# Kernel tuning notes

Measured on AMD Instinct MI355X. Metric: run time of the kernel, lower is better.

## Reference

```python
import jax, jax.numpy as jnp
import numpy as np

HEADS = 16
DIMS = [64, 64, 64, 64]  # [d_att(Q), d_att(K), d_ff(V), d_ff(G)]
EPS = 1e-4
P_POW = 2


def _cdist(Q, K):
    # Euclidean pairwise distance via the norm expansion, like torch.cdist.
    # Q: [h, b, t, d], K: [h, b, t, d] -> [h, b, t, t]
    q2 = jnp.sum(Q * Q, axis=-1)  # [h, b, t]
    k2 = jnp.sum(K * K, axis=-1)  # [h, b, t]
    qk = jnp.einsum('hbtd,hbsd->hbts', Q, K)
    d2 = q2[..., :, None] + k2[..., None, :] - 2.0 * qk
    return jnp.sqrt(jnp.maximum(d2, 0.0))


def setup_inputs() -> dict:
    key = jax.random.key(0)
    ks = jax.random.split(key, 4)
    b, t, d_in = 2, 2048, 1024
    d_proj = HEADS * sum(DIMS)  # 4096
    X = jax.random.normal(ks[0], (b, t, d_in), dtype=jnp.float32)
    W_in = jax.random.normal(ks[1], (d_in, d_proj), dtype=jnp.float32) * (d_in ** -0.5)
    b_in = jnp.zeros((d_proj,), dtype=jnp.float32)
    W_out = jax.random.normal(ks[2], (HEADS * DIMS[2], d_in), dtype=jnp.float32) * ((HEADS * DIMS[2]) ** -0.5)
    b_out = jnp.zeros((d_in,), dtype=jnp.float32)
    return {"X": X, "W_in": W_in, "b_in": b_in, "W_out": W_out, "b_out": b_out}


def reference(X, W_in, b_in, W_out, b_out):
    b, t, _ = X.shape
    # multi-head input projection: [b,t,d_in] -> [h,b,t,sum(DIMS)] -> split
    P = X @ W_in + b_in                       # [b, t, h*sum(DIMS)]
    P = P.reshape(b, t, HEADS, sum(DIMS))
    P = jnp.transpose(P, (2, 0, 1, 3))        # [h, b, t, sum(DIMS)]
    splits = np.cumsum(DIMS)[:-1]
    Q, K, V, G = jnp.split(P, splits, axis=-1)
    # Shepard's attention: inverse-power-distance weights
    W = jnp.power(EPS + _cdist(Q, K), -P_POW)         # [h, b, t, t]
    W = W / (EPS + jnp.sum(W, axis=-1, keepdims=True))
    A = jnp.einsum('hbts,hbse->hbte', W, V)           # [h, b, t, e]
    H = G * A                                          # gating
    H = jnp.transpose(H, (1, 2, 0, 3)).reshape(b, t, HEADS * DIMS[2])
    return H @ W_out + b_out
```

## Files before the change

### kernel.cpp

```cpp
#include <hip/hip_runtime.h>
#include <hip/hip_bf16.h>
#include <cstdint>
#include <cstddef>

typedef __bf16 bf16_t;
typedef __attribute__((ext_vector_type(8))) __bf16 bf16x8;
typedef __attribute__((ext_vector_type(4))) __bf16 bf16x4;
typedef __attribute__((ext_vector_type(4))) float f32x4;
typedef __attribute__((ext_vector_type(16))) float f32x16;
typedef __attribute__((ext_vector_type(4))) unsigned int u32x4;

#define ATT_EPS 1e-4f

__device__ __forceinline__ f32x4 mfma_bf16(bf16x8 a, bf16x8 b, f32x4 c) {
  return __builtin_amdgcn_mfma_f32_16x16x32_bf16(a, b, c, 0, 0, 0);
}
__device__ __forceinline__ f32x16 mfma32(bf16x8 a, bf16x8 b, f32x16 c) {
  return __builtin_amdgcn_mfma_f32_32x32x16_bf16(a, b, c, 0, 0, 0);
}
__device__ __forceinline__ unsigned cvtpk_bf16(float lo, float hi) {
  unsigned r;
  asm("v_cvt_pk_bf16_f32 %0, %1, %2" : "=v"(r) : "v"(lo), "v"(hi));
  return r;
}

#define GLDS16(g, l)                                                          \
  __builtin_amdgcn_global_load_lds(                                           \
      (const __attribute__((address_space(1))) void*)(g),                     \
      (__attribute__((address_space(3))) void*)(l), 16, 0, 0)

__global__ __launch_bounds__(256) void cvt_x_kernel(
    const float* __restrict__ X, bf16_t* __restrict__ Xb, int n8) {
  int i = blockIdx.x * 256 + threadIdx.x;
  if (i >= n8) return;
  f32x4 a = ((const f32x4*)X)[i * 2 + 0];
  f32x4 b = ((const f32x4*)X)[i * 2 + 1];
  bf16x8 o;
  o[0] = (__bf16)a[0]; o[1] = (__bf16)a[1]; o[2] = (__bf16)a[2]; o[3] = (__bf16)a[3];
  o[4] = (__bf16)b[0]; o[5] = (__bf16)b[1]; o[6] = (__bf16)b[2]; o[7] = (__bf16)b[3];
  ((bf16x8*)Xb)[i] = o;
}

__global__ __launch_bounds__(256) void tcvt_kernel(
    const float* __restrict__ W, bf16_t* __restrict__ Wt, int R, int C) {
  __shared__ float T[64][65];
  int tx = threadIdx.x & 63, ty = threadIdx.x >> 6;
  int c0 = blockIdx.x * 64, r0 = blockIdx.y * 64;
#pragma unroll
  for (int i = 0; i < 16; ++i) {
    int rr = ty * 16 + i;
    T[rr][tx] = W[(size_t)(r0 + rr) * C + c0 + tx];
  }
  __syncthreads();
#pragma unroll
  for (int i = 0; i < 16; ++i) {
    int cc = ty * 16 + i;
    Wt[(size_t)(c0 + cc) * R + r0 + tx] = (bf16_t)T[tx][cc];
  }
}

__global__ __launch_bounds__(256) void vt_kernel(
    const bf16_t* __restrict__ P, bf16_t* __restrict__ VtG) {
  __shared__ float T[64][65];
  int h = blockIdx.x;
  int r0 = blockIdx.y * 64;
  int tx = threadIdx.x & 63, ty = threadIdx.x >> 6;
  const bf16_t* src = P + (size_t)r0 * 4096 + h * 256 + 128;
#pragma unroll
  for (int i = 0; i < 16; ++i) {
    int rr = ty * 16 + i;
    T[rr][tx] = (float)src[(size_t)rr * 4096 + tx];
  }
  __syncthreads();
#pragma unroll
  for (int i = 0; i < 16; ++i) {
    int cc = ty * 16 + i;
    VtG[(size_t)(h * 64 + cc) * 4096 + r0 + tx] = (bf16_t)T[tx][cc];
  }
}

template <int OUTF32>
__global__ __launch_bounds__(256, 2) void gemm_kernel(
    const bf16_t* __restrict__ A, const bf16_t* __restrict__ Bt,
    const float* __restrict__ bias, void* __restrict__ Cout,
    int M, int N, int K) {
  __shared__ bf16_t As[2][128 * 64];
  __shared__ bf16_t Bs[2][128 * 64];
  int tid = threadIdx.x, lane = tid & 63, wv = tid >> 6;
  int l15 = lane & 15, lhi = lane >> 4;
  int NT = N >> 7;
  int nwg = gridDim.x;
  int qq = nwg >> 3;
  int swz = (blockIdx.x & 7) * qq + (blockIdx.x >> 3);
  int tm = swz / NT, tn = swz % NT;
  int m0 = tm << 7, n0 = tn << 7;
  int wm = (wv >> 1) << 6, wn = (wv & 1) << 6;
  int KT = K >> 6;

  auto stage = [&](int buf, int kt) {
    int k0 = kt << 6;
#pragma unroll
    for (int s = 0; s < 4; ++s) {
      int t = s * 256 + tid;
      int row = t >> 3, u = t & 7;
      int cc = (u ^ (row & 7)) << 3;
      GLDS16(A + (size_t)(m0 + row) * K + k0 + cc, &As[buf][t * 8]);
    }
#pragma unroll
    for (int s = 0; s < 4; ++s) {
      int t = s * 256 + tid;
      int row = t >> 3, u = t & 7;
      int cc = (u ^ (row & 7)) << 3;
      GLDS16(Bt + (size_t)(n0 + row) * K + k0 + cc, &Bs[buf][t * 8]);
    }
  };

  f32x4 zero = {0.f, 0.f, 0.f, 0.f};
  f32x4 acc[4][4];
#pragma unroll
  for (int ms = 0; ms < 4; ++ms)
#pragma unroll
    for (int ns = 0; ns < 4; ++ns) acc[ms][ns] = zero;

  stage(0, 0);
  __syncthreads();
  int cur = 0;
  for (int kt = 0; kt < KT; ++kt) {
    if (kt + 1 < KT) stage(cur ^ 1, kt + 1);
#pragma unroll
    for (int ks = 0; ks < 2; ++ks) {
      bf16x8 af[4], bfr[4];
#pragma unroll
      for (int ms = 0; ms < 4; ++ms) {
        int row = wm + ms * 16 + l15;
        af[ms] = *(const bf16x8*)&As[cur][row * 64 + (((ks * 4 + lhi) ^ (row & 7)) << 3)];
      }
#pragma unroll
      for (int ns = 0; ns < 4; ++ns) {
        int col = wn + ns * 16 + l15;
        bfr[ns] = *(const bf16x8*)&Bs[cur][col * 64 + (((ks * 4 + lhi) ^ (col & 7)) << 3)];
      }
#pragma unroll
      for (int ms = 0; ms < 4; ++ms)
#pragma unroll
        for (int ns = 0; ns < 4; ++ns)
          acc[ms][ns] = mfma_bf16(af[ms], bfr[ns], acc[ms][ns]);
    }
    __syncthreads();
    cur ^= 1;
  }

#pragma unroll
  for (int ns = 0; ns < 4; ++ns) {
    int col = n0 + wn + ns * 16 + l15;
    float bv = bias[col];
#pragma unroll
    for (int ms = 0; ms < 4; ++ms) {
      int rowb = m0 + wm + ms * 16 + lhi * 4;
#pragma unroll
      for (int r = 0; r < 4; ++r) {
        float v = acc[ms][ns][r] + bv;
        if (OUTF32)
          ((float*)Cout)[(size_t)(rowb + r) * N + col] = v;
        else
          ((bf16_t*)Cout)[(size_t)(rowb + r) * N + col] = (bf16_t)v;
      }
    }
  }
}

__global__ __launch_bounds__(256) void norms_kernel(
    const bf16_t* __restrict__ P, float* __restrict__ Q2, float* __restrict__ K2) {
  int tid = threadIdx.x, lane = tid & 63, wv = tid >> 6;
  int wg = blockIdx.x * 4 + wv;
  int h = wg >> 9, rb = wg & 511;
  int r = rb * 8 + (lane >> 3), ch = lane & 7;
  const bf16_t* base = P + (size_t)r * 4096 + h * 256 + ch * 8;
  bf16x8 qv = *(const bf16x8*)base;
  bf16x8 kv = *(const bf16x8*)(base + 64);
  float sq = 0.f, sk = 0.f;
#pragma unroll
  for (int j = 0; j < 8; ++j) {
    float a = (float)qv[j];
    sq += a * a;
    float c = (float)kv[j];
    sk += c * c;
  }
#pragma unroll
  for (int m = 1; m <= 4; m <<= 1) {
    sq += __shfl_xor(sq, m);
    sk += __shfl_xor(sk, m);
  }
  if (ch == 0) {
    Q2[h * 4096 + r] = sq;
    K2[h * 4096 + r] = sk;
  }
}

__global__ __launch_bounds__(256, 3) void attn_kernel(
    const bf16_t* __restrict__ P, const bf16_t* __restrict__ VtG,
    const float* __restrict__ Q2, const float* __restrict__ K2,
    bf16_t* __restrict__ H) {
  __shared__ bf16_t Ks[128 * 64];
  __shared__ bf16_t Vts[64 * 128];
  __shared__ float invLds[4][32];

  int tid = threadIdx.x, lane = tid & 63, wv = tid >> 6;
  int l31 = lane & 31, hi = lane >> 5, hi4 = hi * 4;
  bool hiSel = (hi != 0);
  int swz = (blockIdx.x & 7) * 64 + (blockIdx.x >> 3);
  int hb = swz >> 4, qt = swz & 15;
  int h = hb >> 1, b = hb & 1;
  int rowbase = b * 2048;
  const bf16_t* Pq = P + (size_t)rowbase * 4096 + h * 256;
  const bf16_t* Pk = Pq + 64;
  const bf16_t* Pg = Pq + 192;
  const bf16_t* Vg = VtG + (size_t)h * 64 * 4096 + rowbase;
  const float* Q2g = Q2 + h * 4096 + rowbase;
  const float* K2g = K2 + h * 4096 + rowbase;
  int q0 = qt * 128 + wv * 32;

  bf16x8 qm[4];
#pragma unroll
  for (int db = 0; db < 4; ++db) {
    bf16x8 q = *(const bf16x8*)(Pq + (size_t)(q0 + l31) * 4096 + db * 16 + hi * 8);
    u32x4 u = *(u32x4*)&q;
    u = (u ^ 0x80008000u) + 0x00800080u;
    qm[db] = *(bf16x8*)&u;
  }
  float q2s = Q2g[q0 + l31];

  f32x16 nacc0, nacc1;
#pragma unroll
  for (int r = 0; r < 16; ++r) { nacc0[r] = 0.f; nacc1[r] = 0.f; }
  float dacc0 = 0.f, dacc1 = 0.f;

  for (int st = 0; st < 16; ++st) {
    int s0 = st * 128;
    __syncthreads();
#pragma unroll
    for (int s4 = 0; s4 < 4; ++s4) {
      int t = s4 * 256 + tid;
      int row = t >> 3, u = t & 7;
      int cc = (u ^ (row & 7)) << 3;
      GLDS16(Pk + (size_t)(s0 + row) * 4096 + cc, &Ks[t * 8]);
    }
#pragma unroll
    for (int s4 = 0; s4 < 4; ++s4) {
      int t = s4 * 256 + tid;
      int row = t >> 4, u = t & 15;
      int cc = (u ^ (row & 7)) << 3;
      GLDS16(Vg + (size_t)row * 4096 + s0 + cc, &Vts[t * 8]);
    }
    __syncthreads();

    const float* K2t = K2g + s0;
#pragma unroll
    for (int sb = 0; sb < 4; ++sb) {
      f32x16 D;
#pragma unroll
      for (int g = 0; g < 4; ++g) {
        f32x4 k2v = *(const f32x4*)(K2t + sb * 32 + g * 8 + hi4);
#pragma unroll
        for (int j = 0; j < 4; ++j) D[g * 4 + j] = k2v[j] + q2s;
      }
#pragma unroll
      for (int db = 0; db < 4; ++db) {
        int srow = sb * 32 + l31;
        bf16x8 kf = *(const bf16x8*)&Ks[srow * 64 + (((db * 2 + hi) ^ (srow & 7)) << 3)];
        D = mfma32(kf, qm[db], D);
      }
      float p[16];
#pragma unroll
      for (int r = 0; r < 16; ++r) {
        float w = __builtin_amdgcn_rcpf(fmaxf(D[r], 1e-12f));
        if (r & 1) dacc1 += w; else dacc0 += w;
        p[r] = w;
      }
      unsigned t01 = cvtpk_bf16(p[0], p[1]),  t23 = cvtpk_bf16(p[2], p[3]);
      unsigned t45 = cvtpk_bf16(p[4], p[5]),  t67 = cvtpk_bf16(p[6], p[7]);
      unsigned t89 = cvtpk_bf16(p[8], p[9]),  tab = cvtpk_bf16(p[10], p[11]);
      unsigned tcd = cvtpk_bf16(p[12], p[13]), tef = cvtpk_bf16(p[14], p[15]);
      unsigned x01 = __shfl_xor(t01, 32), x23 = __shfl_xor(t23, 32);
      unsigned x45 = __shfl_xor(t45, 32), x67 = __shfl_xor(t67, 32);
      unsigned x89 = __shfl_xor(t89, 32), xab = __shfl_xor(tab, 32);
      unsigned xcd = __shfl_xor(tcd, 32), xef = __shfl_xor(tef, 32);
      u32x4 w0v = {hiSel ? x45 : t01, hiSel ? x67 : t23,
                   hiSel ? t45 : x01, hiSel ? t67 : x23};
      u32x4 w1v = {hiSel ? xcd : t89, hiSel ? xef : tab,
                   hiSel ? tcd : x89, hiSel ? tef : xab};
      bf16x8 pa0 = *(bf16x8*)&w0v;
      bf16x8 pa1 = *(bf16x8*)&w1v;
      int e = l31;
      {
        int c0 = ((sb * 4 + 0 + hi) ^ (e & 7)) << 3;
        int c1 = ((sb * 4 + 2 + hi) ^ (e & 7)) << 3;
        bf16x8 vb00 = *(const bf16x8*)&Vts[e * 128 + c0];
        bf16x8 vb01 = *(const bf16x8*)&Vts[(e + 32) * 128 + (((sb * 4 + 0 + hi) ^ ((e + 32) & 7)) << 3)];
        bf16x8 vb10 = *(const bf16x8*)&Vts[e * 128 + c1];
        bf16x8 vb11 = *(const bf16x8*)&Vts[(e + 32) * 128 + (((sb * 4 + 2 + hi) ^ ((e + 32) & 7)) << 3)];
        nacc0 = mfma32(pa0, vb00, nacc0);
        nacc1 = mfma32(pa0, vb01, nacc1);
        nacc0 = mfma32(pa1, vb10, nacc0);
        nacc1 = mfma32(pa1, vb11, nacc1);
      }
    }
  }

  float dacc = dacc0 + dacc1;
  dacc += __shfl_xor(dacc, 32);
  float inv = __builtin_amdgcn_rcpf(ATT_EPS + dacc);
  if (lane < 32) invLds[wv][l31] = inv;
  __builtin_amdgcn_s_waitcnt(0);
#pragma unroll
  for (int r = 0; r < 16; ++r) {
    int q = (r & 3) + 8 * (r >> 2) + hi4;
    int tq = q0 + q;
    float iv = invLds[wv][q];
    float g0 = (float)Pg[(size_t)tq * 4096 + l31];
    float g1 = (float)Pg[(size_t)tq * 4096 + 32 + l31];
    H[(size_t)(rowbase + tq) * 1024 + h * 64 + l31] = (bf16_t)(g0 * nacc0[r] * iv);
    H[(size_t)(rowbase + tq) * 1024 + h * 64 + 32 + l31] = (bf16_t)(g1 * nacc1[r] * iv);
  }
}

extern "C" void kernel_launch(void* const* d_in, const int* in_sizes, int n_in,
                              void* d_out, int out_size, void* d_ws, size_t ws_size,
                              hipStream_t stream) {
  const float* X     = (const float*)d_in[0];
  const float* W_in  = (const float*)d_in[1];
  const float* b_in  = (const float*)d_in[2];
  const float* W_out = (const float*)d_in[3];
  const float* b_out = (const float*)d_in[4];

  char* ws = (char*)d_ws;
  bf16_t* Xb  = (bf16_t*)(ws);
  bf16_t* VtG = (bf16_t*)(ws);
  bf16_t* WbT = (bf16_t*)(ws + ((size_t)8  << 20));
  bf16_t* WoT = (bf16_t*)(ws + ((size_t)16 << 20));
  bf16_t* Pb  = (bf16_t*)(ws + ((size_t)18 << 20));
  bf16_t* Hb  = (bf16_t*)(ws + ((size_t)50 << 20));
  float*  Q2  = (float*) (ws + ((size_t)58 << 20));
  float*  K2  = (float*) (ws + ((size_t)59 << 20));

  cvt_x_kernel<<<2048, 256, 0, stream>>>(X, Xb, 4096 * 1024 / 8);
  tcvt_kernel<<<dim3(64, 16), 256, 0, stream>>>(W_in, WbT, 1024, 4096);
  tcvt_kernel<<<dim3(16, 16), 256, 0, stream>>>(W_out, WoT, 1024, 1024);
  gemm_kernel<0><<<1024, 256, 0, stream>>>(Xb, WbT, b_in, Pb, 4096, 4096, 1024);
  norms_kernel<<<2048, 256, 0, stream>>>(Pb, Q2, K2);
  vt_kernel<<<dim3(16, 64), 256, 0, stream>>>(Pb, VtG);
  attn_kernel<<<512, 256, 0, stream>>>(Pb, VtG, Q2, K2, Hb);
  gemm_kernel<1><<<256, 256, 0, stream>>>(Hb, WoT, b_out, d_out, 4096, 1024, 1024);
}
```

Measured before the change: 157.9 us.

## Split attention key tiles across two wave groups and drop P-fragment shuffles

```diff
diff --git a/kernel.cpp b/kernel.cpp
--- a/kernel.cpp
+++ b/kernel.cpp
@@ -5,7 +5,6 @@
 
 typedef __bf16 bf16_t;
 typedef __attribute__((ext_vector_type(8))) __bf16 bf16x8;
-typedef __attribute__((ext_vector_type(4))) __bf16 bf16x4;
 typedef __attribute__((ext_vector_type(4))) float f32x4;
 typedef __attribute__((ext_vector_type(16))) float f32x16;
 typedef __attribute__((ext_vector_type(4))) unsigned int u32x4;
@@ -72,10 +71,11 @@
     T[rr][tx] = (float)src[(size_t)rr * 4096 + tx];
   }
   __syncthreads();
+  int ptx = (tx & ~15) | ((tx & 3) | ((tx & 4) << 1) | ((tx & 8) >> 1));
 #pragma unroll
   for (int i = 0; i < 16; ++i) {
     int cc = ty * 16 + i;
-    VtG[(size_t)(h * 64 + cc) * 4096 + r0 + tx] = (bf16_t)T[tx][cc];
+    VtG[(size_t)(h * 64 + cc) * 4096 + r0 + ptx] = (bf16_t)T[tx][cc];
   }
 }
 
@@ -197,17 +197,19 @@
   }
 }
 
-__global__ __launch_bounds__(256, 3) void attn_kernel(
+__global__ __launch_bounds__(512, 4) void attn_kernel(
     const bf16_t* __restrict__ P, const bf16_t* __restrict__ VtG,
     const float* __restrict__ Q2, const float* __restrict__ K2,
     bf16_t* __restrict__ H) {
   __shared__ bf16_t Ks[128 * 64];
   __shared__ bf16_t Vts[64 * 128];
+  __shared__ float Comb[4][64][33];
   __shared__ float invLds[4][32];
 
   int tid = threadIdx.x, lane = tid & 63, wv = tid >> 6;
   int l31 = lane & 31, hi = lane >> 5, hi4 = hi * 4;
-  bool hiSel = (hi != 0);
+  int qw = wv & 3, sw = wv >> 2;
+  int sOff = sw * 64;
   int swz = (blockIdx.x & 7) * 64 + (blockIdx.x >> 3);
   int hb = swz >> 4, qt = swz & 15;
   int h = hb >> 1, b = hb & 1;
@@ -218,7 +220,7 @@
   const bf16_t* Vg = VtG + (size_t)h * 64 * 4096 + rowbase;
   const float* Q2g = Q2 + h * 4096 + rowbase;
   const float* K2g = K2 + h * 4096 + rowbase;
-  int q0 = qt * 128 + wv * 32;
+  int q0 = qt * 128 + qw * 32;
 
   bf16x8 qm[4];
 #pragma unroll
@@ -239,34 +241,40 @@
     int s0 = st * 128;
     __syncthreads();
 #pragma unroll
-    for (int s4 = 0; s4 < 4; ++s4) {
-      int t = s4 * 256 + tid;
+    for (int s4 = 0; s4 < 2; ++s4) {
+      int t = s4 * 512 + tid;
       int row = t >> 3, u = t & 7;
       int cc = (u ^ (row & 7)) << 3;
       GLDS16(Pk + (size_t)(s0 + row) * 4096 + cc, &Ks[t * 8]);
     }
 #pragma unroll
-    for (int s4 = 0; s4 < 4; ++s4) {
-      int t = s4 * 256 + tid;
+    for (int s4 = 0; s4 < 2; ++s4) {
+      int t = s4 * 512 + tid;
       int row = t >> 4, u = t & 15;
       int cc = (u ^ (row & 7)) << 3;
       GLDS16(Vg + (size_t)row * 4096 + s0 + cc, &Vts[t * 8]);
     }
+    const float* K2t = K2g + s0 + sOff;
+    f32x4 k2a[4];
+#pragma unroll
+    for (int g = 0; g < 4; ++g) k2a[g] = *(const f32x4*)(K2t + g * 8 + hi4);
     __syncthreads();
 
-    const float* K2t = K2g + s0;
-#pragma unroll
-    for (int sb = 0; sb < 4; ++sb) {
+#pragma unroll
+    for (int sb = 0; sb < 2; ++sb) {
+      int sbase = sOff + sb * 32;
       f32x16 D;
 #pragma unroll
-      for (int g = 0; g < 4; ++g) {
-        f32x4 k2v = *(const f32x4*)(K2t + sb * 32 + g * 8 + hi4);
-#pragma unroll
-        for (int j = 0; j < 4; ++j) D[g * 4 + j] = k2v[j] + q2s;
+      for (int g = 0; g < 4; ++g)
+#pragma unroll
+        for (int j = 0; j < 4; ++j) D[g * 4 + j] = k2a[g][j] + q2s;
+      if (sb == 0) {
+#pragma unroll
+        for (int g = 0; g < 4; ++g) k2a[g] = *(const f32x4*)(K2t + 32 + g * 8 + hi4);
       }
 #pragma unroll
       for (int db = 0; db < 4; ++db) {
-        int srow = sb * 32 + l31;
+        int srow = sbase + l31;
         bf16x8 kf = *(const bf16x8*)&Ks[srow * 64 + (((db * 2 + hi) ^ (srow & 7)) << 3)];
         D = mfma32(kf, qm[db], D);
       }
@@ -277,50 +285,56 @@
         if (r & 1) dacc1 += w; else dacc0 += w;
         p[r] = w;
       }
-      unsigned t01 = cvtpk_bf16(p[0], p[1]),  t23 = cvtpk_bf16(p[2], p[3]);
-      unsigned t45 = cvtpk_bf16(p[4], p[5]),  t67 = cvtpk_bf16(p[6], p[7]);
-      unsigned t89 = cvtpk_bf16(p[8], p[9]),  tab = cvtpk_bf16(p[10], p[11]);
-      unsigned tcd = cvtpk_bf16(p[12], p[13]), tef = cvtpk_bf16(p[14], p[15]);
-      unsigned x01 = __shfl_xor(t01, 32), x23 = __shfl_xor(t23, 32);
-      unsigned x45 = __shfl_xor(t45, 32), x67 = __shfl_xor(t67, 32);
-      unsigned x89 = __shfl_xor(t89, 32), xab = __shfl_xor(tab, 32);
-      unsigned xcd = __shfl_xor(tcd, 32), xef = __shfl_xor(tef, 32);
-      u32x4 w0v = {hiSel ? x45 : t01, hiSel ? x67 : t23,
-                   hiSel ? t45 : x01, hiSel ? t67 : x23};
-      u32x4 w1v = {hiSel ? xcd : t89, hiSel ? xef : tab,
-                   hiSel ? tcd : x89, hiSel ? tef : xab};
+      u32x4 w0v = {cvtpk_bf16(p[0], p[1]), cvtpk_bf16(p[2], p[3]),
+                   cvtpk_bf16(p[4], p[5]), cvtpk_bf16(p[6], p[7])};
+      u32x4 w1v = {cvtpk_bf16(p[8], p[9]), cvtpk_bf16(p[10], p[11]),
+                   cvtpk_bf16(p[12], p[13]), cvtpk_bf16(p[14], p[15])};
       bf16x8 pa0 = *(bf16x8*)&w0v;
       bf16x8 pa1 = *(bf16x8*)&w1v;
       int e = l31;
-      {
-        int c0 = ((sb * 4 + 0 + hi) ^ (e & 7)) << 3;
-        int c1 = ((sb * 4 + 2 + hi) ^ (e & 7)) << 3;
-        bf16x8 vb00 = *(const bf16x8*)&Vts[e * 128 + c0];
-        bf16x8 vb01 = *(const bf16x8*)&Vts[(e + 32) * 128 + (((sb * 4 + 0 + hi) ^ ((e + 32) & 7)) << 3)];
-        bf16x8 vb10 = *(const bf16x8*)&Vts[e * 128 + c1];
-        bf16x8 vb11 = *(const bf16x8*)&Vts[(e + 32) * 128 + (((sb * 4 + 2 + hi) ^ ((e + 32) & 7)) << 3)];
-        nacc0 = mfma32(pa0, vb00, nacc0);
-        nacc1 = mfma32(pa0, vb01, nacc1);
-        nacc0 = mfma32(pa1, vb10, nacc0);
-        nacc1 = mfma32(pa1, vb11, nacc1);
-      }
-    }
-  }
-
-  float dacc = dacc0 + dacc1;
-  dacc += __shfl_xor(dacc, 32);
-  float inv = __builtin_amdgcn_rcpf(ATT_EPS + dacc);
-  if (lane < 32) invLds[wv][l31] = inv;
-  __builtin_amdgcn_s_waitcnt(0);
-#pragma unroll
-  for (int r = 0; r < 16; ++r) {
-    int q = (r & 3) + 8 * (r >> 2) + hi4;
-    int tq = q0 + q;
-    float iv = invLds[wv][q];
-    float g0 = (float)Pg[(size_t)tq * 4096 + l31];
-    float g1 = (float)Pg[(size_t)tq * 4096 + 32 + l31];
-    H[(size_t)(rowbase + tq) * 1024 + h * 64 + l31] = (bf16_t)(g0 * nacc0[r] * iv);
-    H[(size_t)(rowbase + tq) * 1024 + h * 64 + 32 + l31] = (bf16_t)(g1 * nacc1[r] * iv);
+      int ciB = (sOff >> 3) + sb * 4;
+      bf16x8 vb00 = *(const bf16x8*)&Vts[e * 128 + (((ciB + 0 + hi) ^ (e & 7)) << 3)];
+      bf16x8 vb01 = *(const bf16x8*)&Vts[(e + 32) * 128 + (((ciB + 0 + hi) ^ ((e + 32) & 7)) << 3)];
+      bf16x8 vb10 = *(const bf16x8*)&Vts[e * 128 + (((ciB + 2 + hi) ^ (e & 7)) << 3)];
+      bf16x8 vb11 = *(const bf16x8*)&Vts[(e + 32) * 128 + (((ciB + 2 + hi) ^ ((e + 32) & 7)) << 3)];
+      nacc0 = mfma32(pa0, vb00, nacc0);
+      nacc1 = mfma32(pa0, vb01, nacc1);
+      nacc0 = mfma32(pa1, vb10, nacc0);
+      nacc1 = mfma32(pa1, vb11, nacc1);
+    }
+  }
+
+  __syncthreads();
+  if (sw == 1) {
+#pragma unroll
+    for (int r = 0; r < 16; ++r) {
+      Comb[qw][lane][r] = nacc0[r];
+      Comb[qw][lane][16 + r] = nacc1[r];
+    }
+    Comb[qw][lane][32] = dacc0 + dacc1;
+  }
+  __syncthreads();
+  if (sw == 0) {
+    float dacc = dacc0 + dacc1 + Comb[qw][lane][32];
+#pragma unroll
+    for (int r = 0; r < 16; ++r) {
+      nacc0[r] += Comb[qw][lane][r];
+      nacc1[r] += Comb[qw][lane][16 + r];
+    }
+    dacc += __shfl_xor(dacc, 32);
+    float inv = __builtin_amdgcn_rcpf(ATT_EPS + dacc);
+    if (lane < 32) invLds[qw][l31] = inv;
+    __builtin_amdgcn_s_waitcnt(0);
+#pragma unroll
+    for (int r = 0; r < 16; ++r) {
+      int q = (r & 3) + 8 * (r >> 2) + hi4;
+      int tq = q0 + q;
+      float iv = invLds[qw][q];
+      float g0 = (float)Pg[(size_t)tq * 4096 + l31];
+      float g1 = (float)Pg[(size_t)tq * 4096 + 32 + l31];
+      H[(size_t)(rowbase + tq) * 1024 + h * 64 + l31] = (bf16_t)(g0 * nacc0[r] * iv);
+      H[(size_t)(rowbase + tq) * 1024 + h * 64 + 32 + l31] = (bf16_t)(g1 * nacc1[r] * iv);
+    }
   }
 }
 
@@ -349,6 +363,6 @@
   gemm_kernel<0><<<1024, 256, 0, stream>>>(Xb, WbT, b_in, Pb, 4096, 4096, 1024);
   norms_kernel<<<2048, 256, 0, stream>>>(Pb, Q2, K2);
   vt_kernel<<<dim3(16, 64), 256, 0, stream>>>(Pb, VtG);
-  attn_kernel<<<512, 256, 0, stream>>>(Pb, VtG, Q2, K2, Hb);
+  attn_kernel<<<512, 512, 0, stream>>>(Pb, VtG, Q2, K2, Hb);
   gemm_kernel<1><<<256, 256, 0, stream>>>(Hb, WoT, b_out, d_out, 4096, 1024, 1024);
 }
```

New measurement: 145.7 us. -7.7%, faster.
